# Performance work log

Hardware: AMD Instinct MI355X
Metric: run time of the kernel (lower is better)

Reference implementation:

```python
import jax, jax.numpy as jnp
import numpy as np

B, S, M, E, DFF = 4, 2048, 1024, 8, 4096
CAPACITY_FACTOR = 1.25


def setup_inputs() -> dict:
    key = jax.random.key(0)
    k = jax.random.split(key, 5)
    x = jax.random.normal(k[0], (B, S, M), dtype=jnp.float32)
    wg = jax.random.normal(k[1], (M, E), dtype=jnp.float32) * 0.02
    w1 = jax.random.normal(k[2], (E, M, DFF), dtype=jnp.float32) * 0.02
    b1 = jnp.zeros((E, DFF), dtype=jnp.float32)
    w2 = jax.random.normal(k[3], (E, DFF, M), dtype=jnp.float32) * 0.02
    b2 = jnp.zeros((E, M), dtype=jnp.float32)
    return {"x": x, "wg": wg, "w1": w1, "b1": b1, "w2": w2, "b2": b2}


def _top1_gate(tokens, wg, capacity):
    # tokens: [T, M] -> combine_weights [T, E, C], dispatch_mask [T, E, C]
    gates = jax.nn.softmax(tokens @ wg)                      # [T, E]
    expert_idx = jnp.argmax(gates, axis=-1)                  # [T]
    mask1 = jax.nn.one_hot(expert_idx, gates.shape[-1], dtype=gates.dtype)  # [T, E]
    # position of each token within its chosen expert's queue
    pos = jnp.sum(jnp.cumsum(mask1, axis=0) * mask1, axis=-1).astype(jnp.int32) - 1  # [T]
    keep = (pos < capacity).astype(gates.dtype)              # capacity drop
    mask1c = mask1 * keep[:, None]                           # [T, E]
    gates1 = jnp.sum(gates * mask1c, axis=-1)                # chosen prob (0 if dropped)
    loc_oh = jax.nn.one_hot(pos, capacity, dtype=gates.dtype)  # [T, C] (>=C rows -> all 0)
    combine = gates1[:, None, None] * mask1c[:, :, None] * loc_oh[:, None, :]  # [T, E, C]
    dispatch = (combine > 0).astype(tokens.dtype)
    return combine, dispatch


def reference(x, wg, w1, b1, w2, b2):
    d_model = x.shape[-1]
    tokens = x.reshape(-1, d_model)                          # [T, M]
    T = tokens.shape[0]
    num_experts = wg.shape[1]
    capacity = int(CAPACITY_FACTOR * T / num_experts)        # C
    combine, dispatch = _top1_gate(tokens, wg, capacity)
    # dispatch tokens to per-expert buffers: [E, C, M]
    dispatched = jnp.einsum('sec,sm->ecm', dispatch, tokens)
    # per-expert FFN (batched over experts)
    h = jax.nn.relu(jnp.einsum('ecm,emf->ecf', dispatched, w1) + b1[:, None, :])
    expert_out = jnp.einsum('ecf,efm->ecm', h, w2) + b2[:, None, :]
    # combine back to tokens
    combined = jnp.einsum('sec,ecm->sm', combine, expert_out)
    return combined.reshape(x.shape)
```

## Files before the change

### kernel.cpp

```cpp
#include <hip/hip_runtime.h>

#define T_TOKENS 8192
#define MDIM 1024
#define NEXP 8
#define DFF_DIM 4096
#define CAP 1280

typedef __attribute__((ext_vector_type(8))) short short8;
typedef __attribute__((ext_vector_type(4))) float f32x4;

__device__ inline unsigned short f2bf(float f) {
  unsigned u = __float_as_uint(f);
  u = u + 0x7fffu + ((u >> 16) & 1u);
  return (unsigned short)(u >> 16);
}

__device__ __forceinline__ void async_ld16(const void* g, void* l) {
  __builtin_amdgcn_global_load_lds(
      (__attribute__((address_space(1))) void*)const_cast<void*>(g),
      (__attribute__((address_space(3))) void*)l, 16, 0, 0);
}

__global__ __launch_bounds__(64) void gate_kernel(const float* __restrict__ x,
    const float* __restrict__ wg, int* __restrict__ eidx, float* __restrict__ gate)
{
  const int t = blockIdx.x;
  const int lane = threadIdx.x;
  const float* xr = x + (size_t)t * MDIM;
  double acc[NEXP];
  #pragma unroll
  for (int e = 0; e < NEXP; ++e) acc[e] = 0.0;
  for (int m = lane; m < MDIM; m += 64) {
    double xv = (double)xr[m];
    const float* wr = wg + (size_t)m * NEXP;
    #pragma unroll
    for (int e = 0; e < NEXP; ++e) acc[e] += xv * (double)wr[e];
  }
  #pragma unroll
  for (int off = 32; off > 0; off >>= 1) {
    #pragma unroll
    for (int e = 0; e < NEXP; ++e) acc[e] += __shfl_down(acc[e], off);
  }
  if (lane == 0) {
    double mx = acc[0]; int idx = 0;
    #pragma unroll
    for (int e = 1; e < NEXP; ++e) if (acc[e] > mx) { mx = acc[e]; idx = e; }
    double s = 0.0;
    #pragma unroll
    for (int e = 0; e < NEXP; ++e) s += exp(acc[e] - mx);
    eidx[t] = idx;
    gate[t] = (float)(1.0 / s);
  }
}

__global__ __launch_bounds__(1024) void scan_kernel(const int* __restrict__ eidx,
    int* __restrict__ slot_token, int* __restrict__ filled)
{
  __shared__ int hist[16][NEXP];
  __shared__ int wpre[16][NEXP];
  __shared__ int rtot[NEXP];
  __shared__ int base[NEXP];
  const int tid = threadIdx.x;
  const int w = tid >> 6, lane = tid & 63;
  for (int i = tid; i < NEXP * CAP; i += 1024) slot_token[i] = -1;
  if (tid < NEXP) base[tid] = 0;
  __syncthreads();
  const unsigned long long lt = (1ull << lane) - 1ull;
  for (int r = 0; r < T_TOKENS / 1024; ++r) {
    const int t = r * 1024 + tid;
    const int e = eidx[t];
    unsigned long long bal[NEXP];
    #pragma unroll
    for (int ee = 0; ee < NEXP; ++ee) bal[ee] = __ballot(e == ee);
    const int rank = __popcll(bal[e] & lt);
    if (lane < NEXP) hist[w][lane] = __popcll(bal[lane]);
    __syncthreads();
    if (tid < 16 * NEXP) {
      int ww = tid >> 3, ee = tid & 7, s = 0;
      for (int j = 0; j < ww; ++j) s += hist[j][ee];
      wpre[ww][ee] = s;
    }
    if (tid < NEXP) {
      int s = 0;
      for (int j = 0; j < 16; ++j) s += hist[j][tid];
      rtot[tid] = s;
    }
    __syncthreads();
    const int pos = base[e] + wpre[w][e] + rank;
    if (pos < CAP) slot_token[e * CAP + pos] = t;
    __syncthreads();
    if (tid < NEXP) base[tid] += rtot[tid];
    __syncthreads();
  }
  if (tid < NEXP) filled[tid] = (base[tid] < CAP) ? base[tid] : CAP;
}

__global__ __launch_bounds__(256) void dispatch_kernel(const float* __restrict__ x,
    const int* __restrict__ slot_token, unsigned short* __restrict__ Abuf)
{
  const int row = blockIdx.x;
  const int tid = threadIdx.x;
  const int t = slot_token[row];
  unsigned short* dst = Abuf + (size_t)row * MDIM + tid * 4;
  if (t < 0) {
    ushort4 z; z.x = 0; z.y = 0; z.z = 0; z.w = 0;
    *(ushort4*)dst = z;
  } else {
    const float4 v = *(const float4*)(x + (size_t)t * MDIM + tid * 4);
    ushort4 h;
    h.x = f2bf(v.x); h.y = f2bf(v.y); h.z = f2bf(v.z); h.w = f2bf(v.w);
    *(ushort4*)dst = h;
  }
}

template<int R, int Cc>
__global__ __launch_bounds__(256) void transpose_cvt_kernel(
    const float* __restrict__ src, unsigned short* __restrict__ dst)
{
  __shared__ unsigned short tile[64][66];
  const int e = blockIdx.z;
  const int r0 = blockIdx.y * 64;
  const int c0 = blockIdx.x * 64;
  const int t = threadIdx.x;
  const float* S = src + (size_t)e * R * Cc;
  unsigned short* D = dst + (size_t)e * R * Cc;
  const int tr = t >> 4;
  const int tc = (t & 15) * 4;
  #pragma unroll
  for (int i = 0; i < 4; ++i) {
    const int row = i * 16 + tr;
    const float4 v = *(const float4*)(S + (size_t)(r0 + row) * Cc + c0 + tc);
    tile[row][tc + 0] = f2bf(v.x);
    tile[row][tc + 1] = f2bf(v.y);
    tile[row][tc + 2] = f2bf(v.z);
    tile[row][tc + 3] = f2bf(v.w);
  }
  __syncthreads();
  #pragma unroll
  for (int i = 0; i < 4; ++i) {
    const int crow = i * 16 + tr;
    ushort4 o;
    o.x = tile[tc + 0][crow];
    o.y = tile[tc + 1][crow];
    o.z = tile[tc + 2][crow];
    o.w = tile[tc + 3][crow];
    *(ushort4*)(D + (size_t)(c0 + crow) * R + r0 + tc) = o;
  }
}

__global__ __launch_bounds__(512, 2) void gemm1_256(
    const unsigned short* __restrict__ A,
    const unsigned short* __restrict__ Bt,
    const float* __restrict__ bias,
    unsigned short* __restrict__ H,
    const int* __restrict__ filled)
{
  constexpr int N = DFF_DIM;
  constexpr int K = MDIM;
  constexpr int NT = K / 32;
  static_assert(CAP % 256 == 0, "row blocking");

  const int id = blockIdx.x;
  const int wk = (id & 7) * 80 + (id >> 3);
  const int e = wk / 80;
  const int rem = wk % 80;
  const int rowbase = (rem / 16) * 256;
  const int colbase = (rem % 16) * 256;
  if (rowbase >= filled[e]) return;

  __shared__ unsigned short lds[4 * 16384];

  const int tid = threadIdx.x;
  const int lane = tid & 63;
  const int wid = tid >> 6;
  const int wm = wid >> 2;
  const int wn = wid & 3;
  const int qm = lane & 15;
  const int qr = lane >> 4;
  const int swc  = qr ^ ((qm >> 1) & 3);
  const int srcc = (lane & 3) ^ ((lane >> 3) & 3);

  const unsigned short* Ab = A + ((size_t)e * CAP + rowbase) * K;
  const unsigned short* Bb = Bt + ((size_t)e * N + colbase) * K;

  const int srow = wid * 16 + (lane >> 2);
  const unsigned short* aU0 = Ab + (size_t)srow * K + srcc * 8;
  const unsigned short* aU1 = Ab + (size_t)(srow + 128) * K + srcc * 8;
  const unsigned short* bU0 = Bb + (size_t)srow * K + srcc * 8;
  const unsigned short* bU1 = Bb + (size_t)(srow + 128) * K + srcc * 8;

  f32x4 acc[8][4];
  #pragma unroll
  for (int i = 0; i < 8; ++i)
    #pragma unroll
    for (int j = 0; j < 4; ++j)
      #pragma unroll
      for (int r = 0; r < 4; ++r) acc[i][j][r] = 0.0f;

  #define STAGE_A(tt, bb) do { \
    const int k0_ = (tt) * 32; \
    unsigned short* l_ = lds + (bb) * 16384 + wid * 512; \
    async_ld16(aU0 + k0_, l_); \
    async_ld16(aU1 + k0_, l_ + 4096); \
  } while (0)
  #define STAGE_B(tt, bb) do { \
    const int k0_ = (tt) * 32; \
    unsigned short* l_ = lds + (bb) * 16384 + 8192 + wid * 512; \
    async_ld16(bU0 + k0_, l_); \
    async_ld16(bU1 + k0_, l_ + 4096); \
  } while (0)

  STAGE_A(0, 0); STAGE_B(0, 0);
  STAGE_A(1, 1); STAGE_B(1, 1);
  STAGE_A(2, 2); STAGE_B(2, 2);
  asm volatile("s_waitcnt vmcnt(8)" ::: "memory");
  __builtin_amdgcn_s_barrier();

  for (int t = 0; t < NT; ++t) {
    const int buf = t & 3;
    const int pbuf = (t + 3) & 3;
    int ts = t + 3; if (ts >= NT) ts -= NT;
    const unsigned short* Ap = lds + buf * 16384;
    const unsigned short* Bp = Ap + 8192;
    short8 af[4], bfr[4];

    #pragma unroll
    for (int i = 0; i < 4; ++i)
      af[i] = *(const short8*)(Ap + (wm * 128 + i * 16 + qm) * 32 + swc * 8);
    #pragma unroll
    for (int j = 0; j < 4; ++j)
      bfr[j] = *(const short8*)(Bp + (wn * 64 + j * 16 + qm) * 32 + swc * 8);
    STAGE_A(ts, pbuf);
    __builtin_amdgcn_s_barrier();
    asm volatile("s_waitcnt lgkmcnt(0)" ::: "memory");
    __builtin_amdgcn_sched_barrier(0);
    __builtin_amdgcn_s_setprio(1);
    #pragma unroll
    for (int i = 0; i < 4; ++i)
      #pragma unroll
      for (int j = 0; j < 4; ++j)
        acc[i][j] = __builtin_amdgcn_mfma_f32_16x16x32_bf16(af[i], bfr[j], acc[i][j], 0, 0, 0);
    __builtin_amdgcn_s_setprio(0);
    __builtin_amdgcn_s_barrier();

    #pragma unroll
    for (int i = 0; i < 4; ++i)
      af[i] = *(const short8*)(Ap + (wm * 128 + (i + 4) * 16 + qm) * 32 + swc * 8);
    STAGE_B(ts, pbuf);
    __builtin_amdgcn_s_barrier();
    asm volatile("s_waitcnt lgkmcnt(0)" ::: "memory");
    __builtin_amdgcn_sched_barrier(0);
    __builtin_amdgcn_s_setprio(1);
    #pragma unroll
    for (int i = 0; i < 4; ++i)
      #pragma unroll
      for (int j = 0; j < 4; ++j)
        acc[4 + i][j] = __builtin_amdgcn_mfma_f32_16x16x32_bf16(af[i], bfr[j], acc[4 + i][j], 0, 0, 0);
    __builtin_amdgcn_s_setprio(0);
    asm volatile("s_waitcnt vmcnt(8)" ::: "memory");
    __builtin_amdgcn_s_barrier();
  }
  #undef STAGE_A
  #undef STAGE_B

  asm volatile("s_waitcnt vmcnt(0)" ::: "memory");

  float bcol[4];
  #pragma unroll
  for (int j = 0; j < 4; ++j)
    bcol[j] = bias[(size_t)e * N + colbase + wn * 64 + j * 16 + qm];

  #pragma unroll
  for (int i = 0; i < 8; ++i) {
    #pragma unroll
    for (int r = 0; r < 4; ++r) {
      const int row = rowbase + wm * 128 + i * 16 + qr * 4 + r;
      unsigned short* orow = H + ((size_t)e * CAP + row) * N + colbase;
      #pragma unroll
      for (int j = 0; j < 4; ++j) {
        float v = acc[i][j][r] + bcol[j];
        v = v > 0.0f ? v : 0.0f;
        orow[wn * 64 + j * 16 + qm] = f2bf(v);
      }
    }
  }
}

__global__ __launch_bounds__(256) void gemm2_kernel(
    const unsigned short* __restrict__ A, const unsigned short* __restrict__ Bt,
    const float* __restrict__ bias, float* __restrict__ Op,
    const int* __restrict__ slot_token, const float* __restrict__ gate,
    const int* __restrict__ filled)
{
  constexpr int N = MDIM;
  constexpr int K = DFF_DIM;
  const int id = blockIdx.x;
  const int wk = (id & 7) * 80 + (id >> 3);
  const int e = wk / 80;
  const int rem = wk % 80;
  const int colbase = (rem / 10) * 128;
  const int rowbase = (rem % 10) * 128;
  if (rowbase >= filled[e]) return;

  __shared__ unsigned short As[128 * 32];
  __shared__ unsigned short Bs[128 * 32];

  const int tid = threadIdx.x;
  const int lane = tid & 63;
  const int wid = tid >> 6;
  const int wm = (wid >> 1) * 64, wn = (wid & 1) * 64;
  const int qm = lane & 15, qk = (lane >> 4) * 8, qr = lane >> 4;

  const unsigned short* Ab = A + ((size_t)e * CAP + rowbase) * K;
  const unsigned short* Bb = Bt + ((size_t)e * N + colbase) * K;

  const int ldr = wid * 16 + (lane >> 2);
  const int ldk = (lane & 3) * 8;
  const unsigned short* ag = Ab + (size_t)ldr * K + ldk;
  const unsigned short* bg = Bb + (size_t)ldr * K + ldk;
  unsigned short* asw = As + wid * 512;
  unsigned short* bsw = Bs + wid * 512;

  f32x4 acc[4][4];
  #pragma unroll
  for (int i = 0; i < 4; ++i)
    #pragma unroll
    for (int j = 0; j < 4; ++j)
      #pragma unroll
      for (int r = 0; r < 4; ++r) acc[i][j][r] = 0.0f;

  for (int k0 = 0; k0 < K; k0 += 32) {
    __syncthreads();
    async_ld16(ag + k0,                  asw);
    async_ld16(ag + (size_t)64 * K + k0, asw + 2048);
    async_ld16(bg + k0,                  bsw);
    async_ld16(bg + (size_t)64 * K + k0, bsw + 2048);
    __syncthreads();
    short8 af[4], bfr[4];
    #pragma unroll
    for (int i = 0; i < 4; ++i) af[i] = *(const short8*)(As + (wm + i * 16 + qm) * 32 + qk);
    #pragma unroll
    for (int j = 0; j < 4; ++j) bfr[j] = *(const short8*)(Bs + (wn + j * 16 + qm) * 32 + qk);
    #pragma unroll
    for (int i = 0; i < 4; ++i)
      #pragma unroll
      for (int j = 0; j < 4; ++j)
        acc[i][j] = __builtin_amdgcn_mfma_f32_16x16x32_bf16(af[i], bfr[j], acc[i][j], 0, 0, 0);
  }

  float bcol[4];
  #pragma unroll
  for (int j = 0; j < 4; ++j)
    bcol[j] = bias[(size_t)e * N + colbase + wn + j * 16 + qm];

  #pragma unroll
  for (int i = 0; i < 4; ++i) {
    #pragma unroll
    for (int r = 0; r < 4; ++r) {
      const int row = rowbase + wm + i * 16 + qr * 4 + r;
      const int t = slot_token[e * CAP + row];
      if (t >= 0) {
        const float g = gate[t];
        float* orow = Op + (size_t)t * MDIM + colbase;
        #pragma unroll
        for (int j = 0; j < 4; ++j)
          orow[wn + j * 16 + qm] = g * (acc[i][j][r] + bcol[j]);
      }
    }
  }
}

extern "C" void kernel_launch(void* const* d_in, const int* in_sizes, int n_in,
                              void* d_out, int out_size, void* d_ws, size_t ws_size,
                              hipStream_t stream) {
  const float* x  = (const float*)d_in[0];
  const float* wg = (const float*)d_in[1];
  const float* w1 = (const float*)d_in[2];
  const float* b1 = (const float*)d_in[3];
  const float* w2 = (const float*)d_in[4];
  const float* b2 = (const float*)d_in[5];

  char* ws = (char*)d_ws;
  unsigned short* Abuf = (unsigned short*)ws;
  unsigned short* H    = (unsigned short*)(ws + 20971520);
  unsigned short* Wt   = (unsigned short*)(ws + 104857600);
  int*   slot_token    = (int*)(ws + 171966464);
  int*   eidx          = (int*)(ws + 172007424);
  float* gate          = (float*)(ws + 172040192);
  int*   filled        = (int*)(ws + 172072960);

  hipMemsetAsync(d_out, 0, (size_t)out_size * sizeof(float), stream);

  gate_kernel<<<T_TOKENS, 64, 0, stream>>>(x, wg, eidx, gate);
  scan_kernel<<<1, 1024, 0, stream>>>(eidx, slot_token, filled);
  dispatch_kernel<<<NEXP * CAP, 256, 0, stream>>>(x, slot_token, Abuf);

  dim3 gc1(DFF_DIM / 64, MDIM / 64, NEXP);
  transpose_cvt_kernel<MDIM, DFF_DIM><<<gc1, 256, 0, stream>>>(w1, Wt);

  gemm1_256<<<dim3(640), 512, 0, stream>>>(Abuf, Wt, b1, H, filled);

  dim3 gc2(MDIM / 64, DFF_DIM / 64, NEXP);
  transpose_cvt_kernel<DFF_DIM, MDIM><<<gc2, 256, 0, stream>>>(w2, Wt);

  gemm2_kernel<<<dim3(640), 256, 0, stream>>>(H, Wt, b2, (float*)d_out, slot_token, gate, filled);
}
```

Baseline: 575.0 us.

## Rewrite second expert GEMM with 256x128 tiles and 4-stage async LDS pipeline

Replaces the 128x128 single-buffered second GEMM with a 512-thread 256x128-tile kernel that uses a 4-deep ring of LDS buffers filled by async global-to-LDS loads, XOR-swizzled LDS reads, and MFMA phases split in two with raised wave priority. It mirrors the structure already used for the first GEMM. The aim is to hide global load latency, cut LDS bank conflicts, and raise arithmetic intensity per block. In exchange it halves the block count to 320, which lowers parallelism and adds tail waste for partially filled experts. The pipeline also relies on hand-placed waitcnt and barrier ordering.

```diff
diff --git a/kernel.cpp b/kernel.cpp
--- a/kernel.cpp
+++ b/kernel.cpp
@@ -286,85 +286,138 @@
   }
 }
 
-__global__ __launch_bounds__(256) void gemm2_kernel(
-    const unsigned short* __restrict__ A, const unsigned short* __restrict__ Bt,
-    const float* __restrict__ bias, float* __restrict__ Op,
+__global__ __launch_bounds__(512, 2) void gemm2_256(
+    const unsigned short* __restrict__ A,
+    const unsigned short* __restrict__ Bt,
+    const float* __restrict__ bias,
+    float* __restrict__ Op,
     const int* __restrict__ slot_token, const float* __restrict__ gate,
     const int* __restrict__ filled)
 {
   constexpr int N = MDIM;
   constexpr int K = DFF_DIM;
+  constexpr int NT = K / 32;
+
   const int id = blockIdx.x;
-  const int wk = (id & 7) * 80 + (id >> 3);
-  const int e = wk / 80;
-  const int rem = wk % 80;
-  const int colbase = (rem / 10) * 128;
-  const int rowbase = (rem % 10) * 128;
+  const int wk = (id & 7) * 40 + (id >> 3);
+  const int e = wk / 40;
+  const int rem = wk % 40;
+  const int colbase = (rem / 5) * 128;
+  const int rowbase = (rem % 5) * 256;
   if (rowbase >= filled[e]) return;
 
-  __shared__ unsigned short As[128 * 32];
-  __shared__ unsigned short Bs[128 * 32];
+  __shared__ unsigned short lds[4 * 12288];
 
   const int tid = threadIdx.x;
   const int lane = tid & 63;
   const int wid = tid >> 6;
-  const int wm = (wid >> 1) * 64, wn = (wid & 1) * 64;
-  const int qm = lane & 15, qk = (lane >> 4) * 8, qr = lane >> 4;
+  const int wm = wid >> 2;
+  const int wn = wid & 3;
+  const int qm = lane & 15;
+  const int qr = lane >> 4;
+  const int swc  = qr ^ ((qm >> 1) & 3);
+  const int srcc = (lane & 3) ^ ((lane >> 3) & 3);
 
   const unsigned short* Ab = A + ((size_t)e * CAP + rowbase) * K;
   const unsigned short* Bb = Bt + ((size_t)e * N + colbase) * K;
 
-  const int ldr = wid * 16 + (lane >> 2);
-  const int ldk = (lane & 3) * 8;
-  const unsigned short* ag = Ab + (size_t)ldr * K + ldk;
-  const unsigned short* bg = Bb + (size_t)ldr * K + ldk;
-  unsigned short* asw = As + wid * 512;
-  unsigned short* bsw = Bs + wid * 512;
-
-  f32x4 acc[4][4];
-  #pragma unroll
-  for (int i = 0; i < 4; ++i)
-    #pragma unroll
-    for (int j = 0; j < 4; ++j)
+  const int srow = wid * 16 + (lane >> 2);
+  const unsigned short* aU0 = Ab + (size_t)srow * K + srcc * 8;
+  const unsigned short* aU1 = Ab + (size_t)(srow + 128) * K + srcc * 8;
+  const unsigned short* bU0 = Bb + (size_t)srow * K + srcc * 8;
+
+  f32x4 acc[8][2];
+  #pragma unroll
+  for (int i = 0; i < 8; ++i)
+    #pragma unroll
+    for (int j = 0; j < 2; ++j)
       #pragma unroll
       for (int r = 0; r < 4; ++r) acc[i][j][r] = 0.0f;
 
-  for (int k0 = 0; k0 < K; k0 += 32) {
-    __syncthreads();
-    async_ld16(ag + k0,                  asw);
-    async_ld16(ag + (size_t)64 * K + k0, asw + 2048);
-    async_ld16(bg + k0,                  bsw);
-    async_ld16(bg + (size_t)64 * K + k0, bsw + 2048);
-    __syncthreads();
-    short8 af[4], bfr[4];
-    #pragma unroll
-    for (int i = 0; i < 4; ++i) af[i] = *(const short8*)(As + (wm + i * 16 + qm) * 32 + qk);
-    #pragma unroll
-    for (int j = 0; j < 4; ++j) bfr[j] = *(const short8*)(Bs + (wn + j * 16 + qm) * 32 + qk);
-    #pragma unroll
-    for (int i = 0; i < 4; ++i)
-      #pragma unroll
-      for (int j = 0; j < 4; ++j)
+  #define STAGE_A2(tt, bb) do { \
+    const int k0_ = (tt) * 32; \
+    unsigned short* l_ = lds + (bb) * 12288 + wid * 512; \
+    async_ld16(aU0 + k0_, l_); \
+    async_ld16(aU1 + k0_, l_ + 4096); \
+  } while (0)
+  #define STAGE_B2(tt, bb) do { \
+    const int k0_ = (tt) * 32; \
+    unsigned short* l_ = lds + (bb) * 12288 + 8192 + wid * 512; \
+    async_ld16(bU0 + k0_, l_); \
+  } while (0)
+
+  STAGE_A2(0, 0); STAGE_B2(0, 0);
+  STAGE_A2(1, 1); STAGE_B2(1, 1);
+  STAGE_A2(2, 2); STAGE_B2(2, 2);
+  asm volatile("s_waitcnt vmcnt(6)" ::: "memory");
+  __builtin_amdgcn_s_barrier();
+
+  for (int t = 0; t < NT; ++t) {
+    const int buf = t & 3;
+    const int pbuf = (t + 3) & 3;
+    int ts = t + 3; if (ts >= NT) ts -= NT;
+    const unsigned short* Ap = lds + buf * 12288;
+    const unsigned short* Bp = Ap + 8192;
+    short8 af[4], bfr[2];
+
+    #pragma unroll
+    for (int i = 0; i < 4; ++i)
+      af[i] = *(const short8*)(Ap + (wm * 128 + i * 16 + qm) * 32 + swc * 8);
+    #pragma unroll
+    for (int j = 0; j < 2; ++j)
+      bfr[j] = *(const short8*)(Bp + (wn * 32 + j * 16 + qm) * 32 + swc * 8);
+    STAGE_A2(ts, pbuf);
+    __builtin_amdgcn_s_barrier();
+    asm volatile("s_waitcnt lgkmcnt(0)" ::: "memory");
+    __builtin_amdgcn_sched_barrier(0);
+    __builtin_amdgcn_s_setprio(1);
+    #pragma unroll
+    for (int i = 0; i < 4; ++i)
+      #pragma unroll
+      for (int j = 0; j < 2; ++j)
         acc[i][j] = __builtin_amdgcn_mfma_f32_16x16x32_bf16(af[i], bfr[j], acc[i][j], 0, 0, 0);
-  }
-
-  float bcol[4];
-  #pragma unroll
-  for (int j = 0; j < 4; ++j)
-    bcol[j] = bias[(size_t)e * N + colbase + wn + j * 16 + qm];
-
-  #pragma unroll
-  for (int i = 0; i < 4; ++i) {
+    __builtin_amdgcn_s_setprio(0);
+    __builtin_amdgcn_s_barrier();
+
+    #pragma unroll
+    for (int i = 0; i < 4; ++i)
+      af[i] = *(const short8*)(Ap + (wm * 128 + (i + 4) * 16 + qm) * 32 + swc * 8);
+    STAGE_B2(ts, pbuf);
+    __builtin_amdgcn_s_barrier();
+    asm volatile("s_waitcnt lgkmcnt(0)" ::: "memory");
+    __builtin_amdgcn_sched_barrier(0);
+    __builtin_amdgcn_s_setprio(1);
+    #pragma unroll
+    for (int i = 0; i < 4; ++i)
+      #pragma unroll
+      for (int j = 0; j < 2; ++j)
+        acc[4 + i][j] = __builtin_amdgcn_mfma_f32_16x16x32_bf16(af[i], bfr[j], acc[4 + i][j], 0, 0, 0);
+    __builtin_amdgcn_s_setprio(0);
+    asm volatile("s_waitcnt vmcnt(6)" ::: "memory");
+    __builtin_amdgcn_s_barrier();
+  }
+  #undef STAGE_A2
+  #undef STAGE_B2
+
+  asm volatile("s_waitcnt vmcnt(0)" ::: "memory");
+
+  float bcol[2];
+  #pragma unroll
+  for (int j = 0; j < 2; ++j)
+    bcol[j] = bias[(size_t)e * N + colbase + wn * 32 + j * 16 + qm];
+
+  #pragma unroll
+  for (int i = 0; i < 8; ++i) {
     #pragma unroll
     for (int r = 0; r < 4; ++r) {
-      const int row = rowbase + wm + i * 16 + qr * 4 + r;
-      const int t = slot_token[e * CAP + row];
-      if (t >= 0) {
-        const float g = gate[t];
-        float* orow = Op + (size_t)t * MDIM + colbase;
+      const int row = rowbase + wm * 128 + i * 16 + qr * 4 + r;
+      const int tk = slot_token[e * CAP + row];
+      if (tk >= 0) {
+        const float g = gate[tk];
+        float* orow = Op + (size_t)tk * MDIM + colbase;
         #pragma unroll
-        for (int j = 0; j < 4; ++j)
-          orow[wn + j * 16 + qm] = g * (acc[i][j][r] + bcol[j]);
+        for (int j = 0; j < 2; ++j)
+          orow[wn * 32 + j * 16 + qm] = g * (acc[i][j][r] + bcol[j]);
       }
     }
   }
@@ -403,5 +456,5 @@
   dim3 gc2(MDIM / 64, DFF_DIM / 64, NEXP);
   transpose_cvt_kernel<DFF_DIM, MDIM><<<gc2, 256, 0, stream>>>(w2, Wt);
 
-  gemm2_kernel<<<dim3(640), 256, 0, stream>>>(H, Wt, b2, (float*)d_out, slot_token, gate, filled);
-}
+  gemm2_256<<<dim3(320), 512, 0, stream>>>(H, Wt, b2, (float*)d_out, slot_token, gate, filled);
+}
```

New measurement: 608.4 us. +5.8%, slower.

## Unify both expert GEMMs into one templated triple-buffered 128x128 pipelined kernel

Applied to the files above, without the earlier changes.

Replaces the 256x256 gemm1 kernel and the unpipelined, double-sync gemm2 kernel with one templated kernel. It uses 128x128 tiles, a 3-stage async global-to-LDS pipeline with swizzled LDS, and one barrier per k-step. GEMM2 gains prefetch overlap and gets rid of the two __syncthreads per iteration. GEMM1 moves to smaller tiles with more blocks and higher occupancy, at the cost of less data reuse per block.

```diff
diff --git a/kernel.cpp b/kernel.cpp
--- a/kernel.cpp
+++ b/kernel.cpp
@@ -148,35 +148,36 @@
   }
 }
 
-__global__ __launch_bounds__(512, 2) void gemm1_256(
+template<int MODE>
+__global__ __launch_bounds__(256, 3) void gemm_pipe(
     const unsigned short* __restrict__ A,
     const unsigned short* __restrict__ Bt,
     const float* __restrict__ bias,
-    unsigned short* __restrict__ H,
+    void* __restrict__ outp,
+    const int* __restrict__ slot_token, const float* __restrict__ gate,
     const int* __restrict__ filled)
 {
-  constexpr int N = DFF_DIM;
-  constexpr int K = MDIM;
+  constexpr int N = MODE ? MDIM : DFF_DIM;
+  constexpr int K = MODE ? DFF_DIM : MDIM;
   constexpr int NT = K / 32;
-  static_assert(CAP % 256 == 0, "row blocking");
+  constexpr int ROWB = CAP / 128;
+  constexpr int PERE = (N / 128) * ROWB;
 
   const int id = blockIdx.x;
-  const int wk = (id & 7) * 80 + (id >> 3);
-  const int e = wk / 80;
-  const int rem = wk % 80;
-  const int rowbase = (rem / 16) * 256;
-  const int colbase = (rem % 16) * 256;
+  const int wk = (id & 7) * PERE + (id >> 3);
+  const int e = wk / PERE;
+  const int rem = wk % PERE;
+  const int colbase = (rem / ROWB) * 128;
+  const int rowbase = (rem % ROWB) * 128;
   if (rowbase >= filled[e]) return;
 
-  __shared__ unsigned short lds[4 * 16384];
+  __shared__ unsigned short lds[3 * 8192];
 
   const int tid = threadIdx.x;
   const int lane = tid & 63;
   const int wid = tid >> 6;
-  const int wm = wid >> 2;
-  const int wn = wid & 3;
-  const int qm = lane & 15;
-  const int qr = lane >> 4;
+  const int wm = (wid >> 1) * 64, wn = (wid & 1) * 64;
+  const int qm = lane & 15, qr = lane >> 4;
   const int swc  = qr ^ ((qm >> 1) & 3);
   const int srcc = (lane & 3) ^ ((lane >> 3) & 3);
 
@@ -185,53 +186,45 @@
 
   const int srow = wid * 16 + (lane >> 2);
   const unsigned short* aU0 = Ab + (size_t)srow * K + srcc * 8;
-  const unsigned short* aU1 = Ab + (size_t)(srow + 128) * K + srcc * 8;
+  const unsigned short* aU1 = aU0 + (size_t)64 * K;
   const unsigned short* bU0 = Bb + (size_t)srow * K + srcc * 8;
-  const unsigned short* bU1 = Bb + (size_t)(srow + 128) * K + srcc * 8;
-
-  f32x4 acc[8][4];
-  #pragma unroll
-  for (int i = 0; i < 8; ++i)
+  const unsigned short* bU1 = bU0 + (size_t)64 * K;
+
+  f32x4 acc[4][4];
+  #pragma unroll
+  for (int i = 0; i < 4; ++i)
     #pragma unroll
     for (int j = 0; j < 4; ++j)
       #pragma unroll
       for (int r = 0; r < 4; ++r) acc[i][j][r] = 0.0f;
 
-  #define STAGE_A(tt, bb) do { \
+  #define STAGE(tt, bb) do { \
     const int k0_ = (tt) * 32; \
-    unsigned short* l_ = lds + (bb) * 16384 + wid * 512; \
+    unsigned short* l_ = lds + (bb) * 8192 + wid * 512; \
     async_ld16(aU0 + k0_, l_); \
-    async_ld16(aU1 + k0_, l_ + 4096); \
+    async_ld16(aU1 + k0_, l_ + 2048); \
+    async_ld16(bU0 + k0_, l_ + 4096); \
+    async_ld16(bU1 + k0_, l_ + 6144); \
   } while (0)
-  #define STAGE_B(tt, bb) do { \
-    const int k0_ = (tt) * 32; \
-    unsigned short* l_ = lds + (bb) * 16384 + 8192 + wid * 512; \
-    async_ld16(bU0 + k0_, l_); \
-    async_ld16(bU1 + k0_, l_ + 4096); \
-  } while (0)
-
-  STAGE_A(0, 0); STAGE_B(0, 0);
-  STAGE_A(1, 1); STAGE_B(1, 1);
-  STAGE_A(2, 2); STAGE_B(2, 2);
-  asm volatile("s_waitcnt vmcnt(8)" ::: "memory");
+
+  STAGE(0, 0);
+  STAGE(1, 1);
+  asm volatile("s_waitcnt vmcnt(4)" ::: "memory");
   __builtin_amdgcn_s_barrier();
 
+  int buf = 0, nbuf = 1, pbuf = 2;
   for (int t = 0; t < NT; ++t) {
-    const int buf = t & 3;
-    const int pbuf = (t + 3) & 3;
-    int ts = t + 3; if (ts >= NT) ts -= NT;
-    const unsigned short* Ap = lds + buf * 16384;
-    const unsigned short* Bp = Ap + 8192;
+    int ts = t + 2; if (ts >= NT) ts -= NT;
+    const unsigned short* Ap = lds + buf * 8192;
+    const unsigned short* Bp = Ap + 4096;
     short8 af[4], bfr[4];
-
     #pragma unroll
     for (int i = 0; i < 4; ++i)
-      af[i] = *(const short8*)(Ap + (wm * 128 + i * 16 + qm) * 32 + swc * 8);
+      af[i] = *(const short8*)(Ap + (wm + i * 16 + qm) * 32 + swc * 8);
     #pragma unroll
     for (int j = 0; j < 4; ++j)
-      bfr[j] = *(const short8*)(Bp + (wn * 64 + j * 16 + qm) * 32 + swc * 8);
-    STAGE_A(ts, pbuf);
-    __builtin_amdgcn_s_barrier();
+      bfr[j] = *(const short8*)(Bp + (wn + j * 16 + qm) * 32 + swc * 8);
+    STAGE(ts, pbuf);
     asm volatile("s_waitcnt lgkmcnt(0)" ::: "memory");
     __builtin_amdgcn_sched_barrier(0);
     __builtin_amdgcn_s_setprio(1);
@@ -241,130 +234,50 @@
       for (int j = 0; j < 4; ++j)
         acc[i][j] = __builtin_amdgcn_mfma_f32_16x16x32_bf16(af[i], bfr[j], acc[i][j], 0, 0, 0);
     __builtin_amdgcn_s_setprio(0);
+    asm volatile("s_waitcnt vmcnt(4)" ::: "memory");
     __builtin_amdgcn_s_barrier();
-
-    #pragma unroll
-    for (int i = 0; i < 4; ++i)
-      af[i] = *(const short8*)(Ap + (wm * 128 + (i + 4) * 16 + qm) * 32 + swc * 8);
-    STAGE_B(ts, pbuf);
-    __builtin_amdgcn_s_barrier();
-    asm volatile("s_waitcnt lgkmcnt(0)" ::: "memory");
-    __builtin_amdgcn_sched_barrier(0);
-    __builtin_amdgcn_s_setprio(1);
-    #pragma unroll
-    for (int i = 0; i < 4; ++i)
+    const int tmp = buf; buf = nbuf; nbuf = pbuf; pbuf = tmp;
+  }
+  #undef STAGE
+
+  asm volatile("s_waitcnt vmcnt(0)" ::: "memory");
+
+  float bcol[4];
+  #pragma unroll
+  for (int j = 0; j < 4; ++j)
+    bcol[j] = bias[(size_t)e * N + colbase + wn + j * 16 + qm];
+
+  if (MODE == 0) {
+    unsigned short* Hp = (unsigned short*)outp;
+    #pragma unroll
+    for (int i = 0; i < 4; ++i) {
       #pragma unroll
-      for (int j = 0; j < 4; ++j)
-        acc[4 + i][j] = __builtin_amdgcn_mfma_f32_16x16x32_bf16(af[i], bfr[j], acc[4 + i][j], 0, 0, 0);
-    __builtin_amdgcn_s_setprio(0);
-    asm volatile("s_waitcnt vmcnt(8)" ::: "memory");
-    __builtin_amdgcn_s_barrier();
-  }
-  #undef STAGE_A
-  #undef STAGE_B
-
-  asm volatile("s_waitcnt vmcnt(0)" ::: "memory");
-
-  float bcol[4];
-  #pragma unroll
-  for (int j = 0; j < 4; ++j)
-    bcol[j] = bias[(size_t)e * N + colbase + wn * 64 + j * 16 + qm];
-
-  #pragma unroll
-  for (int i = 0; i < 8; ++i) {
-    #pragma unroll
-    for (int r = 0; r < 4; ++r) {
-      const int row = rowbase + wm * 128 + i * 16 + qr * 4 + r;
-      unsigned short* orow = H + ((size_t)e * CAP + row) * N + colbase;
-      #pragma unroll
-      for (int j = 0; j < 4; ++j) {
-        float v = acc[i][j][r] + bcol[j];
-        v = v > 0.0f ? v : 0.0f;
-        orow[wn * 64 + j * 16 + qm] = f2bf(v);
+      for (int r = 0; r < 4; ++r) {
+        const int row = rowbase + wm + i * 16 + qr * 4 + r;
+        unsigned short* orow = Hp + ((size_t)e * CAP + row) * N + colbase;
+        #pragma unroll
+        for (int j = 0; j < 4; ++j) {
+          float v = acc[i][j][r] + bcol[j];
+          v = v > 0.0f ? v : 0.0f;
+          orow[wn + j * 16 + qm] = f2bf(v);
+        }
       }
     }
-  }
-}
-
-__global__ __launch_bounds__(256) void gemm2_kernel(
-    const unsigned short* __restrict__ A, const unsigned short* __restrict__ Bt,
-    const float* __restrict__ bias, float* __restrict__ Op,
-    const int* __restrict__ slot_token, const float* __restrict__ gate,
-    const int* __restrict__ filled)
-{
-  constexpr int N = MDIM;
-  constexpr int K = DFF_DIM;
-  const int id = blockIdx.x;
-  const int wk = (id & 7) * 80 + (id >> 3);
-  const int e = wk / 80;
-  const int rem = wk % 80;
-  const int colbase = (rem / 10) * 128;
-  const int rowbase = (rem % 10) * 128;
-  if (rowbase >= filled[e]) return;
-
-  __shared__ unsigned short As[128 * 32];
-  __shared__ unsigned short Bs[128 * 32];
-
-  const int tid = threadIdx.x;
-  const int lane = tid & 63;
-  const int wid = tid >> 6;
-  const int wm = (wid >> 1) * 64, wn = (wid & 1) * 64;
-  const int qm = lane & 15, qk = (lane >> 4) * 8, qr = lane >> 4;
-
-  const unsigned short* Ab = A + ((size_t)e * CAP + rowbase) * K;
-  const unsigned short* Bb = Bt + ((size_t)e * N + colbase) * K;
-
-  const int ldr = wid * 16 + (lane >> 2);
-  const int ldk = (lane & 3) * 8;
-  const unsigned short* ag = Ab + (size_t)ldr * K + ldk;
-  const unsigned short* bg = Bb + (size_t)ldr * K + ldk;
-  unsigned short* asw = As + wid * 512;
-  unsigned short* bsw = Bs + wid * 512;
-
-  f32x4 acc[4][4];
-  #pragma unroll
-  for (int i = 0; i < 4; ++i)
-    #pragma unroll
-    for (int j = 0; j < 4; ++j)
+  } else {
+    float* Op = (float*)outp;
+    #pragma unroll
+    for (int i = 0; i < 4; ++i) {
       #pragma unroll
-      for (int r = 0; r < 4; ++r) acc[i][j][r] = 0.0f;
-
-  for (int k0 = 0; k0 < K; k0 += 32) {
-    __syncthreads();
-    async_ld16(ag + k0,                  asw);
-    async_ld16(ag + (size_t)64 * K + k0, asw + 2048);
-    async_ld16(bg + k0,                  bsw);
-    async_ld16(bg + (size_t)64 * K + k0, bsw + 2048);
-    __syncthreads();
-    short8 af[4], bfr[4];
-    #pragma unroll
-    for (int i = 0; i < 4; ++i) af[i] = *(const short8*)(As + (wm + i * 16 + qm) * 32 + qk);
-    #pragma unroll
-    for (int j = 0; j < 4; ++j) bfr[j] = *(const short8*)(Bs + (wn + j * 16 + qm) * 32 + qk);
-    #pragma unroll
-    for (int i = 0; i < 4; ++i)
-      #pragma unroll
-      for (int j = 0; j < 4; ++j)
-        acc[i][j] = __builtin_amdgcn_mfma_f32_16x16x32_bf16(af[i], bfr[j], acc[i][j], 0, 0, 0);
-  }
-
-  float bcol[4];
-  #pragma unroll
-  for (int j = 0; j < 4; ++j)
-    bcol[j] = bias[(size_t)e * N + colbase + wn + j * 16 + qm];
-
-  #pragma unroll
-  for (int i = 0; i < 4; ++i) {
-    #pragma unroll
-    for (int r = 0; r < 4; ++r) {
-      const int row = rowbase + wm + i * 16 + qr * 4 + r;
-      const int t = slot_token[e * CAP + row];
-      if (t >= 0) {
-        const float g = gate[t];
-        float* orow = Op + (size_t)t * MDIM + colbase;
-        #pragma unroll
-        for (int j = 0; j < 4; ++j)
-          orow[wn + j * 16 + qm] = g * (acc[i][j][r] + bcol[j]);
+      for (int r = 0; r < 4; ++r) {
+        const int row = rowbase + wm + i * 16 + qr * 4 + r;
+        const int tk = slot_token[e * CAP + row];
+        if (tk >= 0) {
+          const float g = gate[tk];
+          float* orow = Op + (size_t)tk * MDIM + colbase;
+          #pragma unroll
+          for (int j = 0; j < 4; ++j)
+            orow[wn + j * 16 + qm] = g * (acc[i][j][r] + bcol[j]);
+        }
       }
     }
   }
@@ -398,10 +311,12 @@
   dim3 gc1(DFF_DIM / 64, MDIM / 64, NEXP);
   transpose_cvt_kernel<MDIM, DFF_DIM><<<gc1, 256, 0, stream>>>(w1, Wt);
 
-  gemm1_256<<<dim3(640), 512, 0, stream>>>(Abuf, Wt, b1, H, filled);
+  gemm_pipe<0><<<dim3(2560), 256, 0, stream>>>(Abuf, Wt, b1, (void*)H,
+                                               nullptr, nullptr, filled);
 
   dim3 gc2(MDIM / 64, DFF_DIM / 64, NEXP);
   transpose_cvt_kernel<DFF_DIM, MDIM><<<gc2, 256, 0, stream>>>(w2, Wt);
 
-  gemm2_kernel<<<dim3(640), 256, 0, stream>>>(H, Wt, b2, (float*)d_out, slot_token, gate, filled);
-}
+  gemm_pipe<1><<<dim3(640), 256, 0, stream>>>(H, Wt, b2, d_out,
+                                              slot_token, gate, filled);
+}
```

After: 561.1 us. -2.4%, faster.
